# Kernel tuning notes

Hardware: AMD Instinct MI355X
Metric: run time of the kernel (lower is better)

## Reference

```python
import jax, jax.numpy as jnp
import numpy as np

TAU = 2.0
V_TH = 1.0
V_RESET = 0.0
ALPHA = 2.0  # ATan surrogate alpha (spikingjelly default)

@jax.custom_vjp
def spike(x):
    # Heaviside forward, ATan surrogate backward
    return (x >= 0).astype(x.dtype)

def _spike_fwd(x):
    return spike(x), x

def _spike_bwd(x, g):
    pix = (jnp.pi / 2) * ALPHA * x
    return (g * (ALPHA / 2) / (1 + pix * pix),)

spike.defvjp(_spike_fwd, _spike_bwd)

def setup_inputs() -> dict:
    key = jax.random.key(0)
    k1, k2, k3 = jax.random.split(key, 3)
    T, B, I, H = 256, 128, 512, 512
    x = jax.random.normal(k1, (T, B, I), dtype=jnp.float32)
    W = jax.random.normal(k2, (H, I), dtype=jnp.float32) * (1.0 / np.sqrt(I))
    b = jax.random.normal(k3, (H,), dtype=jnp.float32) * 0.01
    return {"x": x, "W": W, "b": b}

def reference(x, W, b):
    # Linear projection over all timesteps at once: (T,B,I) @ (H,I)^T -> (T,B,H)
    h = jnp.einsum('tbi,hi->tbh', x, W) + b

    def step(v, ht):
        # LIFNode, decay_input=False, v_reset=0: charge, fire, hard reset
        v = v - (v - V_RESET) / TAU + ht
        s = spike(v - V_TH)
        s_d = jax.lax.stop_gradient(s)  # detach_reset=True
        v = v * (1.0 - s_d) + V_RESET * s_d
        return v, s

    v0 = jnp.zeros_like(h[0])
    _, spikes = jax.lax.scan(step, v0, h)
    # dropout_p=0 (inference) -> identity; no synapse filter
    return spikes
```

## Files before the change

### kernel.cpp

```cpp
#include <hip/hip_runtime.h>

#define T_STEPS 256
#define B_DIM   128
#define I_DIM   512
#define H_DIM   512
#define M_DIM   (T_STEPS * B_DIM)

#define BM 128
#define BN 128
#define BK 32
#define LDA (BM + 4)
#define LDB (BN + 4)

__global__ __launch_bounds__(256, 2) void gemm_bias_f32(
    const float* __restrict__ A,
    const float* __restrict__ Bw,
    const float* __restrict__ bias,
    float* __restrict__ C)
{
    __shared__ float As[BK][LDA];
    __shared__ float Bs[BK][LDB];

    const int tid = threadIdx.x;
    const int tx  = tid & 15;
    const int ty  = tid >> 4;
    const int m0  = blockIdx.y * BM;
    const int n0  = blockIdx.x * BN;

    float acc[8][8];
    #pragma unroll
    for (int i = 0; i < 8; i++)
        #pragma unroll
        for (int j = 0; j < 8; j++)
            acc[i][j] = 0.0f;

    const int lrow = tid >> 3;
    const int lk   = (tid & 7) * 4;

    const float* Aptr = A  + (size_t)(m0 + lrow) * I_DIM + lk;
    const float* Bptr = Bw + (size_t)(n0 + lrow) * I_DIM + lk;

    for (int k0 = 0; k0 < I_DIM; k0 += BK) {
        float4 av[4], bv[4];
        #pragma unroll
        for (int p = 0; p < 4; p++) {
            av[p] = *(const float4*)(Aptr + (size_t)(p * 32) * I_DIM + k0);
            bv[p] = *(const float4*)(Bptr + (size_t)(p * 32) * I_DIM + k0);
        }

        __syncthreads();

        #pragma unroll
        for (int p = 0; p < 4; p++) {
            const int r = lrow + p * 32;
            As[lk + 0][r] = av[p].x;
            As[lk + 1][r] = av[p].y;
            As[lk + 2][r] = av[p].z;
            As[lk + 3][r] = av[p].w;
            Bs[lk + 0][r] = bv[p].x;
            Bs[lk + 1][r] = bv[p].y;
            Bs[lk + 2][r] = bv[p].z;
            Bs[lk + 3][r] = bv[p].w;
        }

        __syncthreads();

        for (int k = 0; k < BK; k++) {
            float4 a0 = *(const float4*)&As[k][ty * 8];
            float4 a1 = *(const float4*)&As[k][ty * 8 + 4];
            float4 b0 = *(const float4*)&Bs[k][tx * 8];
            float4 b1 = *(const float4*)&Bs[k][tx * 8 + 4];
            float a[8] = {a0.x, a0.y, a0.z, a0.w, a1.x, a1.y, a1.z, a1.w};
            float b[8] = {b0.x, b0.y, b0.z, b0.w, b1.x, b1.y, b1.z, b1.w};
            #pragma unroll
            for (int i = 0; i < 8; i++)
                #pragma unroll
                for (int j = 0; j < 8; j++)
                    acc[i][j] = fmaf(a[i], b[j], acc[i][j]);
        }
    }

    float bcol[8];
    #pragma unroll
    for (int j = 0; j < 8; j++)
        bcol[j] = bias[n0 + tx * 8 + j];

    #pragma unroll
    for (int i = 0; i < 8; i++) {
        const int m = m0 + ty * 8 + i;
        float4 o0, o1;
        o0.x = acc[i][0] + bcol[0];
        o0.y = acc[i][1] + bcol[1];
        o0.z = acc[i][2] + bcol[2];
        o0.w = acc[i][3] + bcol[3];
        o1.x = acc[i][4] + bcol[4];
        o1.y = acc[i][5] + bcol[5];
        o1.z = acc[i][6] + bcol[6];
        o1.w = acc[i][7] + bcol[7];
        float* cp = C + (size_t)m * H_DIM + n0 + tx * 8;
        *(float4*)(cp)     = o0;
        *(float4*)(cp + 4) = o1;
    }
}

#define SCAN_UNROLL 16
__global__ __launch_bounds__(256) void lif_scan(
    const float* __restrict__ h,
    float* __restrict__ out)
{
    const int n   = B_DIM * H_DIM;
    const int idx = blockIdx.x * 256 + threadIdx.x;
    const float* hp = h + idx;
    float* op = out + idx;

    float v = 0.0f;
    for (int t0 = 0; t0 < T_STEPS; t0 += SCAN_UNROLL) {
        float hv[SCAN_UNROLL];
        #pragma unroll
        for (int i = 0; i < SCAN_UNROLL; i++)
            hv[i] = hp[(size_t)(t0 + i) * n];

        float s[SCAN_UNROLL];
        #pragma unroll
        for (int i = 0; i < SCAN_UNROLL; i++) {
            v = 0.5f * v + hv[i];
            const bool fire = (v >= 1.0f);
            s[i] = fire ? 1.0f : 0.0f;
            v    = fire ? 0.0f : v;
        }

        #pragma unroll
        for (int i = 0; i < SCAN_UNROLL; i++)
            op[(size_t)(t0 + i) * n] = s[i];
    }
}

extern "C" void kernel_launch(void* const* d_in, const int* in_sizes, int n_in,
                              void* d_out, int out_size, void* d_ws, size_t ws_size,
                              hipStream_t stream) {
    const float* x = (const float*)d_in[0];
    const float* W = (const float*)d_in[1];
    const float* b = (const float*)d_in[2];
    float* out = (float*)d_out;
    float* h   = (float*)d_ws;

    dim3 grid(H_DIM / BN, M_DIM / BM);
    gemm_bias_f32<<<grid, 256, 0, stream>>>(x, W, b, h);

    lif_scan<<<(B_DIM * H_DIM) / 256, 256, 0, stream>>>(h, out);
}
```

Measured before the change: 317.7 us.

## Widen GEMM tile to 128x256 with XOR-swizzled LDS and register prefetch

Widens the GEMM output tile from 128x128 to 128x256, so each thread accumulates an 8x16 block, raising arithmetic intensity per LDS load. Replaces the padded shared-memory layout with an XOR swizzle to avoid bank conflicts. Issues the next K-tile's global loads after the stores to LDS so they overlap the FMA loop. This raises register pressure (128 accumulators plus 12 prefetched float4s) under launch_bounds(256,2), which risks spills or lower occupancy, and halves the number of blocks in the grid.

```diff
diff --git a/kernel.cpp b/kernel.cpp
--- a/kernel.cpp
+++ b/kernel.cpp
@@ -7,10 +7,9 @@
 #define M_DIM   (T_STEPS * B_DIM)
 
 #define BM 128
-#define BN 128
+#define BN 256
 #define BK 32
-#define LDA (BM + 4)
-#define LDB (BN + 4)
+#define KTILES (I_DIM / BK)
 
 __global__ __launch_bounds__(256, 2) void gemm_bias_f32(
     const float* __restrict__ A,
@@ -18,8 +17,8 @@
     const float* __restrict__ bias,
     float* __restrict__ C)
 {
-    __shared__ float As[BK][LDA];
-    __shared__ float Bs[BK][LDB];
+    __shared__ float As[BK * BM];
+    __shared__ float Bs[BK * BN];
 
     const int tid = threadIdx.x;
     const int tx  = tid & 15;
@@ -27,79 +26,105 @@
     const int m0  = blockIdx.y * BM;
     const int n0  = blockIdx.x * BN;
 
-    float acc[8][8];
+    float acc[8][16];
     #pragma unroll
     for (int i = 0; i < 8; i++)
         #pragma unroll
-        for (int j = 0; j < 8; j++)
+        for (int j = 0; j < 16; j++)
             acc[i][j] = 0.0f;
 
     const int lrow = tid >> 3;
     const int lk   = (tid & 7) * 4;
+    const int q    = tid & 7;
 
     const float* Aptr = A  + (size_t)(m0 + lrow) * I_DIM + lk;
     const float* Bptr = Bw + (size_t)(n0 + lrow) * I_DIM + lk;
 
-    for (int k0 = 0; k0 < I_DIM; k0 += BK) {
-        float4 av[4], bv[4];
+    float4 av[4], bv[8];
+    #pragma unroll
+    for (int p = 0; p < 4; p++)
+        av[p] = *(const float4*)(Aptr + (size_t)(p * 32) * I_DIM);
+    #pragma unroll
+    for (int p = 0; p < 8; p++)
+        bv[p] = *(const float4*)(Bptr + (size_t)(p * 32) * I_DIM);
+
+    for (int kt = 0; kt < KTILES; kt++) {
+        __syncthreads();
+
         #pragma unroll
         for (int p = 0; p < 4; p++) {
-            av[p] = *(const float4*)(Aptr + (size_t)(p * 32) * I_DIM + k0);
-            bv[p] = *(const float4*)(Bptr + (size_t)(p * 32) * I_DIM + k0);
+            const int r    = lrow + p * 32;
+            const int base = (((r >> 2) ^ q) << 2) | (r & 3);
+            As[(lk + 0) * BM + base] = av[p].x;
+            As[(lk + 1) * BM + base] = av[p].y;
+            As[(lk + 2) * BM + base] = av[p].z;
+            As[(lk + 3) * BM + base] = av[p].w;
+        }
+        #pragma unroll
+        for (int p = 0; p < 8; p++) {
+            const int r    = lrow + p * 32;
+            const int base = (((r >> 2) ^ q) << 2) | (r & 3);
+            Bs[(lk + 0) * BN + base] = bv[p].x;
+            Bs[(lk + 1) * BN + base] = bv[p].y;
+            Bs[(lk + 2) * BN + base] = bv[p].z;
+            Bs[(lk + 3) * BN + base] = bv[p].w;
         }
 
         __syncthreads();
 
-        #pragma unroll
-        for (int p = 0; p < 4; p++) {
-            const int r = lrow + p * 32;
-            As[lk + 0][r] = av[p].x;
-            As[lk + 1][r] = av[p].y;
-            As[lk + 2][r] = av[p].z;
-            As[lk + 3][r] = av[p].w;
-            Bs[lk + 0][r] = bv[p].x;
-            Bs[lk + 1][r] = bv[p].y;
-            Bs[lk + 2][r] = bv[p].z;
-            Bs[lk + 3][r] = bv[p].w;
+        if (kt + 1 < KTILES) {
+            const int k0 = (kt + 1) * BK;
+            #pragma unroll
+            for (int p = 0; p < 4; p++)
+                av[p] = *(const float4*)(Aptr + (size_t)(p * 32) * I_DIM + k0);
+            #pragma unroll
+            for (int p = 0; p < 8; p++)
+                bv[p] = *(const float4*)(Bptr + (size_t)(p * 32) * I_DIM + k0);
         }
 
-        __syncthreads();
-
-        for (int k = 0; k < BK; k++) {
-            float4 a0 = *(const float4*)&As[k][ty * 8];
-            float4 a1 = *(const float4*)&As[k][ty * 8 + 4];
-            float4 b0 = *(const float4*)&Bs[k][tx * 8];
-            float4 b1 = *(const float4*)&Bs[k][tx * 8 + 4];
-            float a[8] = {a0.x, a0.y, a0.z, a0.w, a1.x, a1.y, a1.z, a1.w};
-            float b[8] = {b0.x, b0.y, b0.z, b0.w, b1.x, b1.y, b1.z, b1.w};
+        const float4* As4 = (const float4*)As;
+        const float4* Bs4 = (const float4*)Bs;
+        for (int kk = 0; kk < BK; kk += 4) {
+            const int rho = (kk >> 2) & 7;
             #pragma unroll
-            for (int i = 0; i < 8; i++)
+            for (int kj = 0; kj < 4; kj++) {
+                const int k = kk + kj;
+                float4 a0 = As4[k * (BM / 4) + ((ty * 2)     ^ rho)];
+                float4 a1 = As4[k * (BM / 4) + ((ty * 2 + 1) ^ rho)];
+                float4 b0 = Bs4[k * (BN / 4) + ( tx        ^ rho)];
+                float4 b1 = Bs4[k * (BN / 4) + ((16 + tx)  ^ rho)];
+                float4 b2 = Bs4[k * (BN / 4) + ((32 + tx)  ^ rho)];
+                float4 b3 = Bs4[k * (BN / 4) + ((48 + tx)  ^ rho)];
+                float a[8]  = {a0.x, a0.y, a0.z, a0.w, a1.x, a1.y, a1.z, a1.w};
+                float b[16] = {b0.x, b0.y, b0.z, b0.w, b1.x, b1.y, b1.z, b1.w,
+                               b2.x, b2.y, b2.z, b2.w, b3.x, b3.y, b3.z, b3.w};
                 #pragma unroll
-                for (int j = 0; j < 8; j++)
-                    acc[i][j] = fmaf(a[i], b[j], acc[i][j]);
+                for (int i = 0; i < 8; i++)
+                    #pragma unroll
+                    for (int j = 0; j < 16; j++)
+                        acc[i][j] = fmaf(a[i], b[j], acc[i][j]);
+            }
         }
     }
 
-    float bcol[8];
+    float4 bc[4];
     #pragma unroll
-    for (int j = 0; j < 8; j++)
-        bcol[j] = bias[n0 + tx * 8 + j];
+    for (int s = 0; s < 4; s++)
+        bc[s] = *(const float4*)(bias + n0 + 64 * s + tx * 4);
 
     #pragma unroll
     for (int i = 0; i < 8; i++) {
         const int m = m0 + ty * 8 + i;
-        float4 o0, o1;
-        o0.x = acc[i][0] + bcol[0];
-        o0.y = acc[i][1] + bcol[1];
-        o0.z = acc[i][2] + bcol[2];
-        o0.w = acc[i][3] + bcol[3];
-        o1.x = acc[i][4] + bcol[4];
-        o1.y = acc[i][5] + bcol[5];
-        o1.z = acc[i][6] + bcol[6];
-        o1.w = acc[i][7] + bcol[7];
-        float* cp = C + (size_t)m * H_DIM + n0 + tx * 8;
-        *(float4*)(cp)     = o0;
-        *(float4*)(cp + 4) = o1;
+        float* cp = C + (size_t)m * H_DIM + n0 + tx * 4;
+        #pragma unroll
+        for (int s = 0; s < 4; s++) {
+            float4 o;
+            o.x = acc[i][4 * s + 0] + bc[s].x;
+            o.y = acc[i][4 * s + 1] + bc[s].y;
+            o.z = acc[i][4 * s + 2] + bc[s].z;
+            o.w = acc[i][4 * s + 3] + bc[s].w;
+            *(float4*)(cp + 64 * s) = o;
+        }
     }
 }
 
```

Result: slower. 331.5 us (+4.4%).
